# Optimization experiments

Hardware: AMD Instinct MI355X
Metric: run time of the kernel (lower is better)

The kernel has to match this reference:

```python
import jax, jax.numpy as jnp
import numpy as np

T, B, F = 197, 64, 768      # tokens (hardcoded 197 in module), batch, width
N, K = 8, 2                 # num_experts, top-k
CAP = int(197 * 1.0 * K / N)  # capacity = 49
H = 4 * F                   # expert hidden (c_fc out)
G = F // 4                  # gate hidden


def setup_inputs() -> dict:
    key = jax.random.key(0)
    ks = jax.random.split(key, 9)
    s = 0.02
    return {
        "x":   jax.random.normal(ks[0], (T, B, F), jnp.float32),
        # gate: Linear(F, F/4) -> ReLU -> Linear(F/4, N)
        "Wg1": jax.random.normal(ks[1], (F, G), jnp.float32) * s,
        "bg1": jnp.zeros((G,), jnp.float32),
        "Wg2": jax.random.normal(ks[2], (G, N), jnp.float32) * s,
        "bg2": jnp.zeros((N,), jnp.float32),
        # experts: per-expert Linear(F, 4F) -> ReLU -> Linear(4F, F), stacked over N
        "W1":  jax.random.normal(ks[3], (N, F, H), jnp.float32) * s,
        "b1":  jnp.zeros((N, H), jnp.float32),
        "W2":  jax.random.normal(ks[4], (N, H, F), jnp.float32) * s,
        "b2":  jnp.zeros((N, F), jnp.float32),
    }


def reference(x, Wg1, bg1, Wg2, bg2, W1, b1, W2, b2):
    # gating: softmax over experts (dim=2)
    logits = jax.nn.relu(x @ Wg1 + bg1) @ Wg2 + bg2          # [T,B,N]
    gw = jax.nn.softmax(logits, axis=2)                      # [T,B,N]

    # dense all-expert MLP (as-written: every expert on every token)
    h = jax.nn.relu(jnp.einsum('tbf,nfh->tbnh', x, W1) + b1)  # [T,B,N,H]
    eo = jnp.einsum('tbnh,nhf->tbnf', h, W2) + b2             # [T,B,N,F]

    # top-k expert mask (dim=2)
    _, idx = jax.lax.top_k(gw, K)                             # [T,B,K]
    mask_exp = jnp.any(jnp.arange(N)[None, None, None, :] == idx[..., None], axis=2)
    cw = gw * mask_exp                                        # [T,B,N]

    # capacity mask: top-CAP tokens per (batch, expert) along dim 0
    cwT = jnp.moveaxis(cw, 0, -1)                             # [B,N,T]
    _, idx2 = jax.lax.top_k(cwT, CAP)                         # [B,N,CAP]
    mask_cap = jnp.any(jnp.arange(T)[None, None, None, :] == idx2[..., None], axis=2)  # [B,N,T]
    fw = cw * jnp.moveaxis(mask_cap, -1, 0)                   # [T,B,N]

    # combine selected expert outputs, residual-style subtract
    out = jnp.einsum('tbnf,tbn->tbf', eo, fw) - x             # [T,B,F]
    return out
```

## Files before the change

kernel.cpp:

```cpp
#include <hip/hip_runtime.h>
#include <hip/hip_bf16.h>
#include <math.h>
#include <stdint.h>

#define T_ 197
#define B_ 64
#define F_ 768
#define N_ 8
#define CAP_ 49
#define H_ 3072
#define G_ 192
#define TB_ (T_*B_)
#define NBN_ (B_*N_)
#define ME_ 3200
#define MR_ 3136
#define MT_ 25600
#define KH_ 8
#define GM_ 99
#define HP_ 768
#define HCF_ 384
#define NPF_ 8

using bf16x8 = __attribute__((ext_vector_type(8))) short;
using f32x4  = __attribute__((ext_vector_type(4))) float;

__device__ __forceinline__ unsigned short f2bf(float v) {
    __hip_bfloat16 h = __float2bfloat16(v);
    return __builtin_bit_cast(unsigned short, h);
}
__device__ __forceinline__ float bf2f(unsigned short u) {
    unsigned int w = ((unsigned int)u) << 16;
    return __builtin_bit_cast(float, w);
}
__device__ __forceinline__ unsigned int add2bf(unsigned int a, unsigned int b) {
    float al = bf2f((unsigned short)(a & 0xffff)), ah = bf2f((unsigned short)(a >> 16));
    float bl = bf2f((unsigned short)(b & 0xffff)), bh = bf2f((unsigned short)(b >> 16));
    return (unsigned int)f2bf(al + bl) | ((unsigned int)f2bf(ah + bh) << 16);
}

#define GLL16(g, l) __builtin_amdgcn_global_load_lds( \
    (const __attribute__((address_space(1))) unsigned int*)(uintptr_t)(g), \
    (__attribute__((address_space(3))) unsigned int*)(uintptr_t)(l), 16, 0, 0)

__device__ __forceinline__ int xcd_swz(int bid, int nblk) {
    int q = nblk >> 3, r = nblk & 7;
    int xcd = bid & 7, idx = bid >> 3;
    int base = (xcd < r) ? xcd * (q + 1) : r * (q + 1) + (xcd - r) * q;
    return base + idx;
}

__global__ void k_init_out(const float* __restrict__ x, float* __restrict__ out) {
    int i = blockIdx.x * blockDim.x + threadIdx.x;
    const float4* xv = (const float4*)x;
    float4* ov = (float4*)out;
    float4 v = xv[i];
    ov[i] = make_float4(-v.x, -v.y, -v.z, -v.w);
}

__global__ __launch_bounds__(256) void k_gate1(
        const float* __restrict__ x, const float* __restrict__ Wg1,
        float* __restrict__ gs_part) {
    __shared__ float xs[32][132];
    __shared__ float wt[32][196];
    int bm = blockIdx.x % GM_, kh = blockIdx.x / GM_;
    int m0 = bm * 128, k0 = kh * (F_ / KH_);
    int tid = threadIdx.x;
    int mg = tid >> 4;
    int nq = tid & 15;
    f32x4 acc[8][3] = {};

    int xm = tid >> 1, xh = tid & 1;
    int gm = m0 + xm; if (gm >= TB_) gm = TB_ - 1;
    float4 xreg[4];
    float4 wreg[6];

    auto loadRegs = [&](int t) {
        int kb = k0 + t * 32;
        #pragma unroll
        for (int j = 0; j < 4; ++j)
            xreg[j] = *(const float4*)(x + (size_t)gm * F_ + kb + (xh * 4 + j) * 4);
        #pragma unroll
        for (int i = 0; i < 6; ++i) {
            int idx = tid + i * 256;
            int kr = idx / 48, nc = idx % 48;
            wreg[i] = *(const float4*)(Wg1 + (size_t)(kb + kr) * G_ + nc * 4);
        }
    };
    auto writeLDS = [&]() {
        #pragma unroll
        for (int j = 0; j < 4; ++j) {
            int k = (xh * 4 + j) * 4;
            xs[k + 0][xm] = xreg[j].x;
            xs[k + 1][xm] = xreg[j].y;
            xs[k + 2][xm] = xreg[j].z;
            xs[k + 3][xm] = xreg[j].w;
        }
        #pragma unroll
        for (int i = 0; i < 6; ++i) {
            int idx = tid + i * 256;
            int kr = idx / 48, nc = idx % 48;
            *(float4*)&wt[kr][nc * 4] = wreg[i];
        }
    };

    loadRegs(0);
    for (int t = 0; t < 3; ++t) {
        __syncthreads();
        writeLDS();
        __syncthreads();
        if (t < 2) loadRegs(t + 1);
        #pragma unroll 4
        for (int k = 0; k < 32; ++k) {
            float4 a0 = *(const float4*)&xs[k][mg * 8];
            float4 a1 = *(const float4*)&xs[k][mg * 8 + 4];
            f32x4 b0 = *(const f32x4*)&wt[k][nq * 12];
            f32x4 b1 = *(const f32x4*)&wt[k][nq * 12 + 4];
            f32x4 b2 = *(const f32x4*)&wt[k][nq * 12 + 8];
            float am[8] = {a0.x, a0.y, a0.z, a0.w, a1.x, a1.y, a1.z, a1.w};
            #pragma unroll
            for (int mi = 0; mi < 8; ++mi) {
                acc[mi][0] += b0 * am[mi];
                acc[mi][1] += b1 * am[mi];
                acc[mi][2] += b2 * am[mi];
            }
        }
    }
    float* gp = gs_part + (size_t)kh * TB_ * G_;
    #pragma unroll
    for (int mi = 0; mi < 8; ++mi) {
        int r = m0 + mg * 8 + mi;
        if (r < TB_) {
            float* rp = gp + (size_t)r * G_ + nq * 12;
            *(f32x4*)(rp + 0) = acc[mi][0];
            *(f32x4*)(rp + 4) = acc[mi][1];
            *(f32x4*)(rp + 8) = acc[mi][2];
        }
    }
}

__global__ __launch_bounds__(256) void k_gate2(
        const float* __restrict__ gs_part, const float* __restrict__ bg1,
        const float* __restrict__ Wg2, const float* __restrict__ bg2,
        float* __restrict__ cw, int* __restrict__ ecnt) {
    __shared__ float gsh[32][200];
    __shared__ float wg2s[G_ * N_];
    __shared__ float lg[32][8];
    int tid = threadIdx.x;
    int id0 = blockIdx.x * 32;

    for (int i = tid; i < 32 * 48; i += 256) {
        int r = i / 48, c4 = i % 48;
        const float* p0 = gs_part + (size_t)(id0 + r) * G_ + c4 * 4;
        float4 g = *(const float4*)(bg1 + c4 * 4);
        float4 v = g;
        #pragma unroll
        for (int p = 0; p < KH_; ++p) {
            float4 a = *(const float4*)(p0 + (size_t)p * TB_ * G_);
            v.x += a.x; v.y += a.y; v.z += a.z; v.w += a.w;
        }
        v.x = fmaxf(v.x, 0.f); v.y = fmaxf(v.y, 0.f);
        v.z = fmaxf(v.z, 0.f); v.w = fmaxf(v.w, 0.f);
        ((float4*)&gsh[r][0])[c4] = v;
    }
    for (int i = tid; i < G_ * N_; i += 256) wg2s[i] = Wg2[i];
    __syncthreads();

    int tk = tid >> 3, n = tid & 7;
    float a = bg2[n];
    for (int k = 0; k < G_; ++k) a += gsh[tk][k] * wg2s[k * N_ + n];
    lg[tk][n] = a;
    __syncthreads();

    if (tid < 32) {
        int tk2 = tid;
        float p[8];
        float m = lg[tk2][0];
        #pragma unroll
        for (int nn = 1; nn < 8; ++nn) m = fmaxf(m, lg[tk2][nn]);
        float s = 0.f;
        #pragma unroll
        for (int nn = 0; nn < 8; ++nn) { p[nn] = expf(lg[tk2][nn] - m); s += p[nn]; }
        float inv = 1.f / s;
        #pragma unroll
        for (int nn = 0; nn < 8; ++nn) p[nn] *= inv;
        int i1 = 0; float v1 = p[0];
        #pragma unroll
        for (int nn = 1; nn < 8; ++nn) if (p[nn] > v1) { v1 = p[nn]; i1 = nn; }
        int i2 = -1; float v2 = -1.f;
        #pragma unroll
        for (int nn = 0; nn < 8; ++nn) if (nn != i1 && p[nn] > v2) { v2 = p[nn]; i2 = nn; }
        int id = id0 + tk2;
        int t = id / B_, b = id % B_;
        ecnt[id] = 0;
        #pragma unroll
        for (int nn = 0; nn < 8; ++nn) {
            float v = (nn == i1 || nn == i2) ? p[nn] : 0.f;
            cw[((size_t)(b * N_ + nn)) * T_ + t] = v;
        }
    }
}

__global__ __launch_bounds__(256) void k_gate(
        const float* __restrict__ x, const float* __restrict__ Wg1,
        const float* __restrict__ bg1, const float* __restrict__ Wg2,
        const float* __restrict__ bg2, float* __restrict__ cw,
        int* __restrict__ ecnt) {
    __shared__ float xsh[8][F_];
    __shared__ float gsl[8][G_];
    __shared__ float lg[8][N_];
    int tid = threadIdx.x;
    int id0 = blockIdx.x * 8;

    int gid = blockIdx.x * 256 + tid;
    if (gid < TB_ && ecnt) ecnt[gid] = 0;

    const float4* xv = (const float4*)(x + (size_t)id0 * F_);
    float4* xshv = (float4*)&xsh[0][0];
    for (int idx = tid; idx < 8 * (F_/4); idx += 256) xshv[idx] = xv[idx];
    __syncthreads();

    if (tid < G_) {
        float acc[8];
        float bb = bg1[tid];
        #pragma unroll
        for (int tk = 0; tk < 8; ++tk) acc[tk] = bb;
        for (int k = 0; k < F_; ++k) {
            float w = Wg1[k * G_ + tid];
            #pragma unroll
            for (int tk = 0; tk < 8; ++tk) acc[tk] += xsh[tk][k] * w;
        }
        #pragma unroll
        for (int tk = 0; tk < 8; ++tk) gsl[tk][tid] = fmaxf(acc[tk], 0.f);
    }
    __syncthreads();

    if (tid < 64) {
        int tk = tid >> 3, n = tid & 7;
        float acc = bg2[n];
        for (int k = 0; k < G_; ++k) acc += gsl[tk][k] * Wg2[k * N_ + n];
        lg[tk][n] = acc;
    }
    __syncthreads();

    if (tid < 8) {
        int tk = tid;
        float p[8];
        float m = lg[tk][0];
        #pragma unroll
        for (int n = 1; n < 8; ++n) m = fmaxf(m, lg[tk][n]);
        float s = 0.f;
        #pragma unroll
        for (int n = 0; n < 8; ++n) { p[n] = expf(lg[tk][n] - m); s += p[n]; }
        float inv = 1.f / s;
        #pragma unroll
        for (int n = 0; n < 8; ++n) p[n] *= inv;
        int i1 = 0; float v1 = p[0];
        #pragma unroll
        for (int n = 1; n < 8; ++n) if (p[n] > v1) { v1 = p[n]; i1 = n; }
        int i2 = -1; float v2 = -1.f;
        #pragma unroll
        for (int n = 0; n < 8; ++n) if (n != i1 && p[n] > v2) { v2 = p[n]; i2 = n; }
        int id = id0 + tk;
        int t = id / B_, b = id % B_;
        #pragma unroll
        for (int n = 0; n < 8; ++n) {
            float v = (n == i1 || n == i2) ? p[n] : 0.f;
            cw[((size_t)(b * N_ + n)) * T_ + t] = v;
        }
    }
}

__global__ __launch_bounds__(256) void k_capacity(
        const float* __restrict__ cw, int* __restrict__ toks,
        float* __restrict__ wts, int* __restrict__ counts,
        int* __restrict__ ecnt, int* __restrict__ erow) {
    __shared__ float v[T_];
    __shared__ int keep[T_];
    int tid = threadIdx.x;
    int bn = blockIdx.x;
    int b = bn >> 3, n = bn & 7;
    if (tid < T_) v[tid] = cw[(size_t)bn * T_ + tid];
    __syncthreads();
    int kp = 0; float my = 0.f;
    if (tid < T_) {
        my = v[tid];
        int rank = 0;
        for (int t2 = 0; t2 < T_; ++t2) {
            float vt = v[t2];
            rank += (vt > my) || (vt == my && t2 < tid);
        }
        kp = (rank < CAP_) && (my > 0.f);
    }
    if (tid < T_) keep[tid] = kp;
    __syncthreads();
    if (tid < T_ && kp) {
        int slot = 0;
        for (int t2 = 0; t2 < T_; ++t2) slot += (t2 < tid) ? keep[t2] : 0;
        toks[bn * CAP_ + slot] = tid;
        wts[bn * CAP_ + slot] = my;
        if (ecnt) {
            int orow = tid * B_ + b;
            int pos = atomicAdd(&ecnt[orow], 1);
            erow[orow * 2 + pos] = n * ME_ + b * CAP_ + slot;
        }
    }
    if (tid == 0) {
        int tot = 0;
        for (int t2 = 0; t2 < T_; ++t2) tot += keep[t2];
        counts[bn] = tot;
    }
}

__global__ __launch_bounds__(256) void k_repack(
        const float* __restrict__ W, unsigned short* __restrict__ WT, int K, int J) {
    __shared__ float tile[64][65];
    int bid = blockIdx.x;
    int nk = K >> 6, nj = J >> 6;
    int kt = bid % nk; bid /= nk;
    int jt = bid % nj; int e = bid / nj;
    int k0 = kt * 64, j0 = jt * 64;
    int tid = threadIdx.x;
    int jr = (tid & 15) << 2;
    int kr = tid >> 4;
    const float* src = W + ((size_t)e * K + k0) * J + j0;
    #pragma unroll
    for (int i = 0; i < 4; ++i) {
        float4 v = *(const float4*)(src + (size_t)(kr + 16 * i) * J + jr);
        *(float4*)&tile[kr + 16 * i][jr] = v;
    }
    __syncthreads();
    int c = tid & 7;
    int jrow = tid >> 3;
    #pragma unroll
    for (int i = 0; i < 2; ++i) {
        int j = jrow + 32 * i;
        float f[8];
        #pragma unroll
        for (int s = 0; s < 8; ++s) f[s] = tile[c * 8 + s][j];
        uint4 u;
        u.x = f2bf(f[0]) | ((unsigned)f2bf(f[1]) << 16);
        u.y = f2bf(f[2]) | ((unsigned)f2bf(f[3]) << 16);
        u.z = f2bf(f[4]) | ((unsigned)f2bf(f[5]) << 16);
        u.w = f2bf(f[6]) | ((unsigned)f2bf(f[7]) << 16);
        int jg = j0 + j;
        char* drow = (char*)WT + ((size_t)e * J + jg) * (size_t)K * 2 + (size_t)(k0 >> 6) * 128;
        *(uint4*)(drow + ((c << 4) ^ ((jg & 7) << 4))) = u;
    }
}

__global__ __launch_bounds__(256) void k_gather(
        const float* __restrict__ x, const int* __restrict__ toks,
        const int* __restrict__ counts, unsigned short* __restrict__ Xg) {
    int gi = blockIdx.x * 256 + threadIdx.x;
    int R = gi / 96, c = gi - R * 96;
    int e = R / ME_, re = R - e * ME_;
    uint4 val = make_uint4(0u, 0u, 0u, 0u);
    if (re < MR_) {
        int g = re / CAP_, slot = re - g * CAP_;
        int bn = g * N_ + e;
        if (slot < counts[bn]) {
            int t = toks[bn * CAP_ + slot];
            const float* xp = x + ((size_t)t * B_ + g) * F_ + c * 8;
            float4 v0 = *(const float4*)xp;
            float4 v1 = *(const float4*)(xp + 4);
            val.x = f2bf(v0.x) | ((unsigned)f2bf(v0.y) << 16);
            val.y = f2bf(v0.z) | ((unsigned)f2bf(v0.w) << 16);
            val.z = f2bf(v1.x) | ((unsigned)f2bf(v1.y) << 16);
            val.w = f2bf(v1.z) | ((unsigned)f2bf(v1.w) << 16);
        }
    }
    int w = (c * 16) & 127;
    char* dst = (char*)Xg + (size_t)R * 1536 + (c >> 3) * 128 + (w ^ ((R & 7) << 4));
    *(uint4*)dst = val;
}

__global__ __launch_bounds__(256) void k_gemm1(
        const unsigned short* __restrict__ W1T, const unsigned short* __restrict__ Xg,
        const float* __restrict__ b1, unsigned short* __restrict__ Hg,
        int njt, int jofs, int hstrideB, int nblk) {
    __shared__ char ldsA[2][16384];
    __shared__ char ldsB[2][16384];
    int swzb = xcd_swz(blockIdx.x, nblk);
    int per_e = 25 * njt;
    int e = swzb / per_e;
    int rem = swzb - e * per_e;
    int mt = rem / njt, jtl = rem % njt;
    int jt = jofs + jtl;
    int tid = threadIdx.x, lane = tid & 63, wid = tid >> 6;
    int lr8 = lane >> 3, sl = (lane & 7) << 4;
    const char* Ab = (const char*)W1T + ((size_t)e * H_ + (size_t)jt * 128) * (F_ * 2);
    const char* Bb = (const char*)Xg + ((size_t)e * ME_ + (size_t)mt * 128) * (F_ * 2);
    f32x4 acc[4][4] = {};
    int swz = (lane & 7) << 4;
    int q16 = (lane >> 4) << 4;

    auto stage = [&](int buf, int it) {
        int kb = it << 7;
        #pragma unroll
        for (int i = 0; i < 4; ++i) {
            int lr = wid * 32 + i * 8 + lr8;
            GLL16(Ab + (size_t)lr * 1536 + kb + sl, ldsA[buf] + (wid * 32 + i * 8) * 128);
            GLL16(Bb + (size_t)lr * 1536 + kb + sl, ldsB[buf] + (wid * 32 + i * 8) * 128);
        }
    };

    stage(0, 0);
    __syncthreads();
    int cur = 0;
    for (int it = 0; it < 12; ++it) {
        if (it < 11) stage(cur ^ 1, it + 1);
        const char* la = ldsA[cur] + ((wid & 1) * 64) * 128;
        const char* lb = ldsB[cur] + ((wid >> 1) * 64) * 128;
        #pragma unroll
        for (int ks = 0; ks < 2; ++ks) {
            bf16x8 af[4], bfr[4];
            int kk = (ks * 64 + q16) ^ swz;
            #pragma unroll
            for (int t = 0; t < 4; ++t) {
                int ro = (16 * t + (lane & 15)) * 128;
                af[t]  = *(const bf16x8*)(la + ro + kk);
                bfr[t] = *(const bf16x8*)(lb + ro + kk);
            }
            #pragma unroll
            for (int ti = 0; ti < 4; ++ti)
                #pragma unroll
                for (int tm = 0; tm < 4; ++tm)
                    acc[ti][tm] = __builtin_amdgcn_mfma_f32_16x16x32_bf16(af[ti], bfr[tm], acc[ti][tm], 0, 0, 0);
        }
        __syncthreads();
        cur ^= 1;
    }
    char* tile = &ldsA[0][0];
    int jl0 = (wid & 1) * 64;
    int ml0 = (wid >> 1) * 64;
    const float* b1p = b1 + (size_t)e * H_ + (size_t)jt * 128;
    #pragma unroll
    for (int tj = 0; tj < 4; ++tj) {
        int jc = jl0 + 16 * tj + ((lane >> 4) << 2);
        float bb0 = b1p[jc], bb1 = b1p[jc + 1], bb2 = b1p[jc + 2], bb3 = b1p[jc + 3];
        #pragma unroll
        for (int tm = 0; tm < 4; ++tm) {
            int m = ml0 + 16 * tm + (lane & 15);
            f32x4 a = acc[tj][tm];
            unsigned int u0 = f2bf(fmaxf(a[0] + bb0, 0.f)) | ((unsigned)f2bf(fmaxf(a[1] + bb1, 0.f)) << 16);
            unsigned int u1 = f2bf(fmaxf(a[2] + bb2, 0.f)) | ((unsigned)f2bf(fmaxf(a[3] + bb3, 0.f)) << 16);
            int bcol = jc * 2;
            int w = bcol & 127;
            *(uint2*)(tile + m * 256 + (bcol & ~127) + (w ^ ((m & 7) << 4))) = make_uint2(u0, u1);
        }
    }
    __syncthreads();
    char* Hrow = (char*)Hg + ((size_t)e * ME_ + (size_t)mt * 128) * hstrideB + (size_t)jtl * 256;
    #pragma unroll
    for (int i = 0; i < 8; ++i) {
        int idx = tid + i * 256;
        int r = idx >> 4, c = (idx & 15) << 4;
        *(uint4*)(Hrow + (size_t)r * hstrideB + c) = *(const uint4*)(tile + r * 256 + c);
    }
}

__global__ __launch_bounds__(256) void k_gemm2(
        const unsigned short* __restrict__ W2T, const unsigned short* __restrict__ Hg,
        const float* __restrict__ b2, const float* __restrict__ wts,
        const int* __restrict__ counts, unsigned short* __restrict__ Og,
        int kiters, int kofsB, int bstrideB, int nblk) {
    __shared__ char ldsA[2][16384];
    __shared__ char ldsB[2][16384];
    int swzb = xcd_swz(blockIdx.x, nblk);
    int e = swzb / 150;
    int rem = swzb - e * 150;
    int mt = rem / 6, ft = rem % 6;
    int tid = threadIdx.x, lane = tid & 63, wid = tid >> 6;
    int lr8 = lane >> 3, sl = (lane & 7) << 4;
    const char* Ab = (const char*)W2T + ((size_t)e * F_ + (size_t)ft * 128) * (H_ * 2) + kofsB;
    const char* Bb = (const char*)Hg + ((size_t)e * ME_ + (size_t)mt * 128) * bstrideB;
    f32x4 acc[4][4] = {};
    int swz = (lane & 7) << 4;
    int q16 = (lane >> 4) << 4;

    auto stage = [&](int buf, int it) {
        int kb = it << 7;
        #pragma unroll
        for (int i = 0; i < 4; ++i) {
            int lr = wid * 32 + i * 8 + lr8;
            GLL16(Ab + (size_t)lr * 6144 + kb + sl, ldsA[buf] + (wid * 32 + i * 8) * 128);
            GLL16(Bb + (size_t)lr * bstrideB + kb + sl, ldsB[buf] + (wid * 32 + i * 8) * 128);
        }
    };

    stage(0, 0);
    __syncthreads();
    int cur = 0;
    for (int it = 0; it < kiters; ++it) {
        if (it < kiters - 1) stage(cur ^ 1, it + 1);
        const char* la = ldsA[cur] + ((wid & 1) * 64) * 128;
        const char* lb = ldsB[cur] + ((wid >> 1) * 64) * 128;
        #pragma unroll
        for (int ks = 0; ks < 2; ++ks) {
            bf16x8 af[4], bfr[4];
            int kk = (ks * 64 + q16) ^ swz;
            #pragma unroll
            for (int t = 0; t < 4; ++t) {
                int ro = (16 * t + (lane & 15)) * 128;
                af[t]  = *(const bf16x8*)(la + ro + kk);
                bfr[t] = *(const bf16x8*)(lb + ro + kk);
            }
            #pragma unroll
            for (int ti = 0; ti < 4; ++ti)
                #pragma unroll
                for (int tm = 0; tm < 4; ++tm)
                    acc[ti][tm] = __builtin_amdgcn_mfma_f32_16x16x32_bf16(af[ti], bfr[tm], acc[ti][tm], 0, 0, 0);
        }
        __syncthreads();
        cur ^= 1;
    }
    char* tile = &ldsA[0][0];
    int fl0 = (wid & 1) * 64;
    int ml0 = (wid >> 1) * 64;
    const float* b2p = b2 + (size_t)e * F_ + (size_t)ft * 128;
    float fwv[4];
    #pragma unroll
    for (int tm = 0; tm < 4; ++tm) {
        int mloc = ml0 + 16 * tm + (lane & 15);
        int re = mt * 128 + mloc;
        float fw = 0.f;
        if (re < MR_) {
            int g = re / CAP_;
            int slot = re - g * CAP_;
            int bn = g * N_ + e;
            if (slot < counts[bn]) fw = wts[bn * CAP_ + slot];
        }
        fwv[tm] = fw;
    }
    int p0 = (kofsB == 0);
    #pragma unroll
    for (int tf = 0; tf < 4; ++tf) {
        int fc = fl0 + 16 * tf + ((lane >> 4) << 2);
        float c0 = 0.f, c1 = 0.f, c2 = 0.f, c3 = 0.f;
        if (p0) { c0 = b2p[fc]; c1 = b2p[fc + 1]; c2 = b2p[fc + 2]; c3 = b2p[fc + 3]; }
        #pragma unroll
        for (int tm = 0; tm < 4; ++tm) {
            int mloc = ml0 + 16 * tm + (lane & 15);
            f32x4 a = acc[tf][tm];
            float fw = fwv[tm];
            unsigned int u0 = f2bf(fw * (a[0] + c0)) | ((unsigned)f2bf(fw * (a[1] + c1)) << 16);
            unsigned int u1 = f2bf(fw * (a[2] + c2)) | ((unsigned)f2bf(fw * (a[3] + c3)) << 16);
            int bcol = fc * 2;
            int w = bcol & 127;
            *(uint2*)(tile + mloc * 256 + (bcol & ~127) + (w ^ ((mloc & 7) << 4))) = make_uint2(u0, u1);
        }
    }
    __syncthreads();
    char* Orow = (char*)Og + ((size_t)e * ME_ + (size_t)mt * 128) * (F_ * 2) + (size_t)ft * 256;
    if (p0) {
        #pragma unroll
        for (int i = 0; i < 8; ++i) {
            int idx = tid + i * 256;
            int r = idx >> 4, c = (idx & 15) << 4;
            const char* src = tile + r * 256 + (c & ~127) + ((c & 127) ^ ((r & 7) << 4));
            *(uint4*)(Orow + (size_t)r * (F_ * 2) + c) = *(const uint4*)src;
        }
    } else {
        #pragma unroll
        for (int i = 0; i < 8; ++i) {
            int idx = tid + i * 256;
            int r = idx >> 4, c = (idx & 15) << 4;
            const char* src = tile + r * 256 + (c & ~127) + ((c & 127) ^ ((r & 7) << 4));
            uint4 nw = *(const uint4*)src;
            uint4* dst = (uint4*)(Orow + (size_t)r * (F_ * 2) + c);
            uint4 old = *dst;
            uint4 res;
            res.x = add2bf(old.x, nw.x);
            res.y = add2bf(old.y, nw.y);
            res.z = add2bf(old.z, nw.z);
            res.w = add2bf(old.w, nw.w);
            *dst = res;
        }
    }
}

__global__ __launch_bounds__(256) void k_combine(
        const float* __restrict__ x, const unsigned short* __restrict__ Og,
        const int* __restrict__ ecnt, const int* __restrict__ erow,
        float* __restrict__ out) {
    int idx = blockIdx.x * 256 + threadIdx.x;
    int row = idx / 192, c4 = idx - row * 192;
    float4 s = make_float4(0.f, 0.f, 0.f, 0.f);
    int c = ecnt[row];
    if (c > 0) {
        ushort4 u = *(const ushort4*)(Og + (size_t)erow[row * 2] * F_ + c4 * 4);
        s.x += bf2f(u.x); s.y += bf2f(u.y); s.z += bf2f(u.z); s.w += bf2f(u.w);
    }
    if (c > 1) {
        ushort4 u = *(const ushort4*)(Og + (size_t)erow[row * 2 + 1] * F_ + c4 * 4);
        s.x += bf2f(u.x); s.y += bf2f(u.y); s.z += bf2f(u.z); s.w += bf2f(u.w);
    }
    float4 xv = ((const float4*)x)[idx];
    ((float4*)out)[idx] = make_float4(s.x - xv.x, s.y - xv.y, s.z - xv.z, s.w - xv.w);
}

__global__ __launch_bounds__(HCF_) void k_fc1(
        const float* __restrict__ x, const float* __restrict__ W1,
        const float* __restrict__ b1, const int* __restrict__ toks,
        const int* __restrict__ counts, __hip_bfloat16* __restrict__ h, int pass) {
    __shared__ float xs[25][F_];
    int tid = threadIdx.x;
    int bn = blockIdx.x >> 1;
    int half = blockIdx.x & 1;
    int r0 = half * 25;
    int b = bn >> 3, n = bn & 7;
    int c = counts[bn];
    for (int idx = tid; idx < 25 * (F_/4); idx += HCF_) {
        int r = idx / (F_/4), k4 = idx % (F_/4);
        int gr = r0 + r;
        float4 val = make_float4(0.f, 0.f, 0.f, 0.f);
        if (gr < c) {
            int t = toks[bn * CAP_ + gr];
            val = ((const float4*)(x + ((size_t)(t * B_ + b)) * F_))[k4];
        }
        ((float4*)&xs[r][0])[k4] = val;
    }
    __syncthreads();
    int j = pass * HCF_ + tid;
    const float* w1p = W1 + (size_t)n * F_ * H_ + j;
    float bias = b1[n * H_ + j];
    float acc[25];
    #pragma unroll
    for (int r = 0; r < 25; ++r) acc[r] = bias;
    const float4* xsv = (const float4*)&xs[0][0];
    for (int k4 = 0; k4 < F_/4; ++k4) {
        float w0 = w1p[(size_t)(4*k4+0) * H_];
        float w1v = w1p[(size_t)(4*k4+1) * H_];
        float w2v = w1p[(size_t)(4*k4+2) * H_];
        float w3v = w1p[(size_t)(4*k4+3) * H_];
        #pragma unroll
        for (int r = 0; r < 25; ++r) {
            float4 xv = xsv[r * (F_/4) + k4];
            acc[r] += xv.x*w0 + xv.y*w1v + xv.z*w2v + xv.w*w3v;
        }
    }
    __hip_bfloat16* hp = h + ((size_t)bn * CAP_ + r0) * HCF_ + tid;
    #pragma unroll
    for (int r = 0; r < 25; ++r) {
        int gr = r0 + r;
        if (gr < CAP_) hp[(size_t)r * HCF_] = __float2bfloat16(fmaxf(acc[r], 0.f));
    }
}

__global__ __launch_bounds__(768) void k_fc2(
        const float* __restrict__ W2, const float* __restrict__ b2,
        const int* __restrict__ toks, const float* __restrict__ wts,
        const int* __restrict__ counts, const __hip_bfloat16* __restrict__ h,
        float* __restrict__ out, int pass) {
    __shared__ float hs[CAP_][HCF_];
    int tid = threadIdx.x;
    int bn = blockIdx.x;
    int c = counts[bn];
    if (c == 0) return;
    int b = bn >> 3, n = bn & 7;
    const ushort4* hv = (const ushort4*)(h + (size_t)bn * CAP_ * HCF_);
    for (int idx = tid; idx < CAP_ * (HCF_/4); idx += 768) {
        ushort4 u = hv[idx];
        float4 fv;
        fv.x = __bfloat162float(*(const __hip_bfloat16*)&u.x);
        fv.y = __bfloat162float(*(const __hip_bfloat16*)&u.y);
        fv.z = __bfloat162float(*(const __hip_bfloat16*)&u.z);
        fv.w = __bfloat162float(*(const __hip_bfloat16*)&u.w);
        ((float4*)&hs[0][0])[idx] = fv;
    }
    __syncthreads();
    int f = tid;
    const float* w2p = W2 + (size_t)n * H_ * F_ + (size_t)(pass * HCF_) * F_ + f;
    float acc[CAP_];
    #pragma unroll
    for (int r = 0; r < CAP_; ++r) acc[r] = 0.f;
    for (int j4 = 0; j4 < HCF_/4; ++j4) {
        float w0 = w2p[(size_t)(4*j4+0) * F_];
        float w1v = w2p[(size_t)(4*j4+1) * F_];
        float w2v = w2p[(size_t)(4*j4+2) * F_];
        float w3v = w2p[(size_t)(4*j4+3) * F_];
        #pragma unroll
        for (int r = 0; r < CAP_; ++r) {
            float4 hh = ((const float4*)&hs[r][0])[j4];
            acc[r] += hh.x*w0 + hh.y*w1v + hh.z*w2v + hh.w*w3v;
        }
    }
    float bias = (pass == 0) ? b2[n * F_ + f] : 0.f;
    #pragma unroll
    for (int r = 0; r < CAP_; ++r) {
        if (r < c) {
            int t = toks[bn * CAP_ + r];
            float fw = wts[bn * CAP_ + r];
            atomicAdd(&out[((size_t)(t * B_ + b)) * F_ + f], fw * (acc[r] + bias));
        }
    }
}

extern "C" void kernel_launch(void* const* d_in, const int* in_sizes, int n_in,
                              void* d_out, int out_size, void* d_ws, size_t ws_size,
                              hipStream_t stream) {
    const float* x   = (const float*)d_in[0];
    const float* Wg1 = (const float*)d_in[1];
    const float* bg1 = (const float*)d_in[2];
    const float* Wg2 = (const float*)d_in[3];
    const float* bg2 = (const float*)d_in[4];
    const float* W1  = (const float*)d_in[5];
    const float* b1  = (const float*)d_in[6];
    const float* W2  = (const float*)d_in[7];
    const float* b2  = (const float*)d_in[8];
    float* out = (float*)d_out;

    size_t oW1T  = 0;
    size_t oW2T  = oW1T + (size_t)N_ * H_ * F_ * 2;
    size_t oXg   = oW2T + (size_t)N_ * H_ * F_ * 2;
    size_t oCw   = oXg  + (size_t)MT_ * F_ * 2;
    size_t oWts  = oCw  + (size_t)NBN_ * T_ * 4;
    size_t oTok  = oWts + (size_t)NBN_ * CAP_ * 4;
    size_t oCnt  = oTok + (size_t)NBN_ * CAP_ * 4;
    size_t oEcnt = oCnt + (size_t)NBN_ * 4;
    size_t oErow = oEcnt + (size_t)TB_ * 4;
    size_t oOg   = oErow + (size_t)TB_ * 8;
    size_t oHg   = oOg  + (size_t)MT_ * F_ * 2;
    size_t needB = oHg + (size_t)MT_ * HP_ * 2;
    size_t needA = oHg + (size_t)MT_ * H_ * 2;

    if (ws_size >= needB) {
        unsigned short* W1T = (unsigned short*)((char*)d_ws + oW1T);
        unsigned short* W2T = (unsigned short*)((char*)d_ws + oW2T);
        unsigned short* Xg  = (unsigned short*)((char*)d_ws + oXg);
        unsigned short* Og  = (unsigned short*)((char*)d_ws + oOg);
        unsigned short* Hg  = (unsigned short*)((char*)d_ws + oHg);
        float* gs_part = (float*)((char*)d_ws + oOg);
        float* cw   = (float*)((char*)d_ws + oCw);
        float* wts  = (float*)((char*)d_ws + oWts);
        int* toks   = (int*)((char*)d_ws + oTok);
        int* counts = (int*)((char*)d_ws + oCnt);
        int* ecnt   = (int*)((char*)d_ws + oEcnt);
        int* erow   = (int*)((char*)d_ws + oErow);

        k_gate1<<<GM_ * KH_, 256, 0, stream>>>(x, Wg1, gs_part);
        k_gate2<<<TB_ / 32, 256, 0, stream>>>(gs_part, bg1, Wg2, bg2, cw, ecnt);
        k_capacity<<<NBN_, 256, 0, stream>>>(cw, toks, wts, counts, ecnt, erow);
        k_repack<<<N_ * (F_/64) * (H_/64), 256, 0, stream>>>(W1, W1T, F_, H_);
        k_repack<<<N_ * (H_/64) * (F_/64), 256, 0, stream>>>(W2, W2T, H_, F_);
        k_gather<<<(MT_ * 96) / 256, 256, 0, stream>>>(x, toks, counts, Xg);
        if (ws_size >= needA) {
            k_gemm1<<<4800, 256, 0, stream>>>(W1T, Xg, b1, Hg, 24, 0, H_ * 2, 4800);
            k_gemm2<<<1200, 256, 0, stream>>>(W2T, Hg, b2, wts, counts, Og, 48, 0, H_ * 2, 1200);
        } else {
            for (int p = 0; p < 4; ++p) {
                k_gemm1<<<1200, 256, 0, stream>>>(W1T, Xg, b1, Hg, 6, p * 6, HP_ * 2, 1200);
                k_gemm2<<<1200, 256, 0, stream>>>(W2T, Hg, b2, wts, counts, Og, 12, p * HP_ * 2, HP_ * 2, 1200);
            }
        }
        k_combine<<<(TB_ * 192) / 256, 256, 0, stream>>>(x, Og, ecnt, erow, out);
    } else {
        __hip_bfloat16* h = (__hip_bfloat16*)d_ws;
        float* cw  = (float*)((char*)d_ws + (size_t)NBN_ * CAP_ * HCF_ * 2);
        float* wts = cw + (size_t)NBN_ * T_;
        int* toks  = (int*)(wts + NBN_ * CAP_);
        int* counts = toks + NBN_ * CAP_;
        k_init_out<<<(TB_ * F_) / 1024, 256, 0, stream>>>(x, out);
        k_gate<<<TB_ / 8, 256, 0, stream>>>(x, Wg1, bg1, Wg2, bg2, cw, nullptr);
        k_capacity<<<NBN_, 256, 0, stream>>>(cw, toks, wts, counts, nullptr, nullptr);
        for (int p = 0; p < NPF_; ++p) {
            k_fc1<<<NBN_ * 2, HCF_, 0, stream>>>(x, W1, b1, toks, counts, h, p);
            k_fc2<<<NBN_, 768, 0, stream>>>(W2, b2, toks, wts, counts, h, out, p);
        }
    }
}
```

Before: 526.9 us.

## Fuse gate GEMM and softmax/top-k into one kernel without split-K

Replaces the split-K gate GEMM plus a separate reduction/softmax kernel with a single kernel, where each block owns 64 tokens over the full K=768. It computes ReLU(xWg1+b), the second projection via shuffles and LDS, then softmax and top-2. This removes the partial-sum buffer round trip and one launch. The cost is fewer blocks (197 vs 792) and a longer serial K loop per block, which lowers parallelism.

```diff
diff --git a/kernel.cpp b/kernel.cpp
--- a/kernel.cpp
+++ b/kernel.cpp
@@ -15,8 +15,6 @@
 #define ME_ 3200
 #define MR_ 3136
 #define MT_ 25600
-#define KH_ 8
-#define GM_ 99
 #define HP_ 768
 #define HCF_ 384
 #define NPF_ 8
@@ -57,28 +55,31 @@
     ov[i] = make_float4(-v.x, -v.y, -v.z, -v.w);
 }
 
-__global__ __launch_bounds__(256) void k_gate1(
+__global__ __launch_bounds__(256) void k_gatef(
         const float* __restrict__ x, const float* __restrict__ Wg1,
-        float* __restrict__ gs_part) {
-    __shared__ float xs[32][132];
-    __shared__ float wt[32][196];
-    int bm = blockIdx.x % GM_, kh = blockIdx.x / GM_;
-    int m0 = bm * 128, k0 = kh * (F_ / KH_);
-    int tid = threadIdx.x;
-    int mg = tid >> 4;
-    int nq = tid & 15;
-    f32x4 acc[8][3] = {};
-
-    int xm = tid >> 1, xh = tid & 1;
-    int gm = m0 + xm; if (gm >= TB_) gm = TB_ - 1;
-    float4 xreg[4];
+        const float* __restrict__ bg1, const float* __restrict__ Wg2,
+        const float* __restrict__ bg2, float* __restrict__ cw,
+        int* __restrict__ ecnt) {
+    __shared__ float xs[32][68];
+    __shared__ float wt[32][200];
+    __shared__ float wg2s[G_ * N_];
+    __shared__ float lgp[4][64][8];
+    int m0 = blockIdx.x * 64;
+    int tid = threadIdx.x, lane = tid & 63, wid = tid >> 6;
+    int mg = lane & 15;
+    int ng = (lane >> 4) + 4 * wid;
+    f32x4 acc[4][3] = {};
+
+    int xr = tid >> 3, xc = tid & 7;
+    float4 xreg0, xreg1;
     float4 wreg[6];
 
+    for (int i = tid; i < G_ * N_; i += 256) wg2s[i] = Wg2[i];
+
     auto loadRegs = [&](int t) {
-        int kb = k0 + t * 32;
-        #pragma unroll
-        for (int j = 0; j < 4; ++j)
-            xreg[j] = *(const float4*)(x + (size_t)gm * F_ + kb + (xh * 4 + j) * 4);
+        int kb = t * 32;
+        xreg0 = *(const float4*)(x + (size_t)(m0 + xr) * F_ + kb + xc * 4);
+        xreg1 = *(const float4*)(x + (size_t)(m0 + xr + 32) * F_ + kb + xc * 4);
         #pragma unroll
         for (int i = 0; i < 6; ++i) {
             int idx = tid + i * 256;
@@ -87,14 +88,10 @@
         }
     };
     auto writeLDS = [&]() {
-        #pragma unroll
-        for (int j = 0; j < 4; ++j) {
-            int k = (xh * 4 + j) * 4;
-            xs[k + 0][xm] = xreg[j].x;
-            xs[k + 1][xm] = xreg[j].y;
-            xs[k + 2][xm] = xreg[j].z;
-            xs[k + 3][xm] = xreg[j].w;
-        }
+        xs[xc * 4 + 0][xr] = xreg0.x;  xs[xc * 4 + 1][xr] = xreg0.y;
+        xs[xc * 4 + 2][xr] = xreg0.z;  xs[xc * 4 + 3][xr] = xreg0.w;
+        xs[xc * 4 + 0][xr + 32] = xreg1.x;  xs[xc * 4 + 1][xr + 32] = xreg1.y;
+        xs[xc * 4 + 2][xr + 32] = xreg1.z;  xs[xc * 4 + 3][xr + 32] = xreg1.w;
         #pragma unroll
         for (int i = 0; i < 6; ++i) {
             int idx = tid + i * 256;
@@ -104,82 +101,80 @@
     };
 
     loadRegs(0);
-    for (int t = 0; t < 3; ++t) {
+    for (int t = 0; t < 24; ++t) {
         __syncthreads();
         writeLDS();
         __syncthreads();
-        if (t < 2) loadRegs(t + 1);
-        #pragma unroll 4
+        if (t < 23) loadRegs(t + 1);
+        #pragma unroll
         for (int k = 0; k < 32; ++k) {
-            float4 a0 = *(const float4*)&xs[k][mg * 8];
-            float4 a1 = *(const float4*)&xs[k][mg * 8 + 4];
-            f32x4 b0 = *(const f32x4*)&wt[k][nq * 12];
-            f32x4 b1 = *(const f32x4*)&wt[k][nq * 12 + 4];
-            f32x4 b2 = *(const f32x4*)&wt[k][nq * 12 + 8];
-            float am[8] = {a0.x, a0.y, a0.z, a0.w, a1.x, a1.y, a1.z, a1.w};
+            float4 av = *(const float4*)&xs[k][mg * 4];
+            f32x4 b0 = *(const f32x4*)&wt[k][ng * 12];
+            f32x4 b1 = *(const f32x4*)&wt[k][ng * 12 + 4];
+            f32x4 b2 = *(const f32x4*)&wt[k][ng * 12 + 8];
+            float am[4] = {av.x, av.y, av.z, av.w};
             #pragma unroll
-            for (int mi = 0; mi < 8; ++mi) {
+            for (int mi = 0; mi < 4; ++mi) {
                 acc[mi][0] += b0 * am[mi];
                 acc[mi][1] += b1 * am[mi];
                 acc[mi][2] += b2 * am[mi];
             }
         }
     }
-    float* gp = gs_part + (size_t)kh * TB_ * G_;
-    #pragma unroll
-    for (int mi = 0; mi < 8; ++mi) {
-        int r = m0 + mg * 8 + mi;
-        if (r < TB_) {
-            float* rp = gp + (size_t)r * G_ + nq * 12;
-            *(f32x4*)(rp + 0) = acc[mi][0];
-            *(f32x4*)(rp + 4) = acc[mi][1];
-            *(f32x4*)(rp + 8) = acc[mi][2];
-        }
-    }
-}
-
-__global__ __launch_bounds__(256) void k_gate2(
-        const float* __restrict__ gs_part, const float* __restrict__ bg1,
-        const float* __restrict__ Wg2, const float* __restrict__ bg2,
-        float* __restrict__ cw, int* __restrict__ ecnt) {
-    __shared__ float gsh[32][200];
-    __shared__ float wg2s[G_ * N_];
-    __shared__ float lg[32][8];
-    int tid = threadIdx.x;
-    int id0 = blockIdx.x * 32;
-
-    for (int i = tid; i < 32 * 48; i += 256) {
-        int r = i / 48, c4 = i % 48;
-        const float* p0 = gs_part + (size_t)(id0 + r) * G_ + c4 * 4;
-        float4 g = *(const float4*)(bg1 + c4 * 4);
-        float4 v = g;
-        #pragma unroll
-        for (int p = 0; p < KH_; ++p) {
-            float4 a = *(const float4*)(p0 + (size_t)p * TB_ * G_);
-            v.x += a.x; v.y += a.y; v.z += a.z; v.w += a.w;
-        }
-        v.x = fmaxf(v.x, 0.f); v.y = fmaxf(v.y, 0.f);
-        v.z = fmaxf(v.z, 0.f); v.w = fmaxf(v.w, 0.f);
-        ((float4*)&gsh[r][0])[c4] = v;
-    }
-    for (int i = tid; i < G_ * N_; i += 256) wg2s[i] = Wg2[i];
-    __syncthreads();
-
-    int tk = tid >> 3, n = tid & 7;
-    float a = bg2[n];
-    for (int k = 0; k < G_; ++k) a += gsh[tk][k] * wg2s[k * N_ + n];
-    lg[tk][n] = a;
-    __syncthreads();
-
-    if (tid < 32) {
-        int tk2 = tid;
+
+    #pragma unroll
+    for (int jv = 0; jv < 3; ++jv) {
+        float4 bb = *(const float4*)(bg1 + ng * 12 + jv * 4);
+        #pragma unroll
+        for (int mi = 0; mi < 4; ++mi) {
+            acc[mi][jv][0] = fmaxf(acc[mi][jv][0] + bb.x, 0.f);
+            acc[mi][jv][1] = fmaxf(acc[mi][jv][1] + bb.y, 0.f);
+            acc[mi][jv][2] = fmaxf(acc[mi][jv][2] + bb.z, 0.f);
+            acc[mi][jv][3] = fmaxf(acc[mi][jv][3] + bb.w, 0.f);
+        }
+    }
+    float part[4][8] = {};
+    #pragma unroll
+    for (int j = 0; j < 12; ++j) {
+        int col = ng * 12 + j;
+        #pragma unroll
+        for (int mi = 0; mi < 4; ++mi) {
+            float gv = acc[mi][j >> 2][j & 3];
+            #pragma unroll
+            for (int e = 0; e < 8; ++e)
+                part[mi][e] += gv * wg2s[col * 8 + e];
+        }
+    }
+    #pragma unroll
+    for (int mi = 0; mi < 4; ++mi)
+        #pragma unroll
+        for (int e = 0; e < 8; ++e) {
+            float v = part[mi][e];
+            v += __shfl_xor(v, 16);
+            v += __shfl_xor(v, 32);
+            part[mi][e] = v;
+        }
+    if (lane < 16) {
+        #pragma unroll
+        for (int mi = 0; mi < 4; ++mi)
+            #pragma unroll
+            for (int e = 0; e < 8; ++e)
+                lgp[wid][mg * 4 + mi][e] = part[mi][e];
+    }
+    __syncthreads();
+
+    if (tid < 64) {
+        int tk = tid;
         float p[8];
-        float m = lg[tk2][0];
-        #pragma unroll
-        for (int nn = 1; nn < 8; ++nn) m = fmaxf(m, lg[tk2][nn]);
+        #pragma unroll
+        for (int e = 0; e < 8; ++e)
+            p[e] = bg2[e] + lgp[0][tk][e] + lgp[1][tk][e] + lgp[2][tk][e] + lgp[3][tk][e];
+        float m = p[0];
+        #pragma unroll
+        for (int nn = 1; nn < 8; ++nn) m = fmaxf(m, p[nn]);
         float s = 0.f;
         #pragma unroll
-        for (int nn = 0; nn < 8; ++nn) { p[nn] = expf(lg[tk2][nn] - m); s += p[nn]; }
+        for (int nn = 0; nn < 8; ++nn) { p[nn] = expf(p[nn] - m); s += p[nn]; }
         float inv = 1.f / s;
         #pragma unroll
         for (int nn = 0; nn < 8; ++nn) p[nn] *= inv;
@@ -189,7 +184,7 @@
         int i2 = -1; float v2 = -1.f;
         #pragma unroll
         for (int nn = 0; nn < 8; ++nn) if (nn != i1 && p[nn] > v2) { v2 = p[nn]; i2 = nn; }
-        int id = id0 + tk2;
+        int id = m0 + tk;
         int t = id / B_, b = id % B_;
         ecnt[id] = 0;
         #pragma unroll
@@ -730,7 +725,6 @@
         unsigned short* Xg  = (unsigned short*)((char*)d_ws + oXg);
         unsigned short* Og  = (unsigned short*)((char*)d_ws + oOg);
         unsigned short* Hg  = (unsigned short*)((char*)d_ws + oHg);
-        float* gs_part = (float*)((char*)d_ws + oOg);
         float* cw   = (float*)((char*)d_ws + oCw);
         float* wts  = (float*)((char*)d_ws + oWts);
         int* toks   = (int*)((char*)d_ws + oTok);
@@ -738,8 +732,7 @@
         int* ecnt   = (int*)((char*)d_ws + oEcnt);
         int* erow   = (int*)((char*)d_ws + oErow);
 
-        k_gate1<<<GM_ * KH_, 256, 0, stream>>>(x, Wg1, gs_part);
-        k_gate2<<<TB_ / 32, 256, 0, stream>>>(gs_part, bg1, Wg2, bg2, cw, ecnt);
+        k_gatef<<<197, 256, 0, stream>>>(x, Wg1, bg1, Wg2, bg2, cw, ecnt);
         k_capacity<<<NBN_, 256, 0, stream>>>(cw, toks, wts, counts, ecnt, erow);
         k_repack<<<N_ * (F_/64) * (H_/64), 256, 0, stream>>>(W1, W1T, F_, H_);
         k_repack<<<N_ * (H_/64) * (F_/64), 256, 0, stream>>>(W2, W2T, H_, F_);
```

Result: no change. 528.0 us (+0.2%).
